# Optimization experiments

Measured on AMD Instinct MI355X. Metric: run time of the kernel, lower is better.

The kernel has to match this reference:

```python
import jax, jax.numpy as jnp
import numpy as np

N, E, H = 50000, 800000, 128
NUM_NC = 40
NUM_LAYERS = 3


def setup_inputs() -> dict:
    key = jax.random.key(0)
    ks = jax.random.split(key, 16)
    s = 1.0 / np.sqrt(H)
    inp = {
        "x": jax.random.normal(ks[0], (N, H), jnp.float32),
        "edge_index": jax.random.randint(ks[1], (2, E), 0, N, jnp.int64),
        "na_alphas": 0.001 * jax.random.normal(ks[2], (3, 4), jnp.float32),
        "sc_alphas": 0.001 * jax.random.normal(ks[3], (2, 2), jnp.float32),
        "la_alphas": 0.001 * jax.random.normal(ks[4], (1, 3), jnp.float32),
        "lin1_W": s * jax.random.normal(ks[5], (H, H), jnp.float32),
        "lin1_b": jnp.zeros((H,), jnp.float32),
        "gcn_W": s * jax.random.normal(ks[6], (3, H, H), jnp.float32),
        "gcn_b": jnp.zeros((3, H), jnp.float32),
        "sage_Ws": s * jax.random.normal(ks[7], (3, H, H), jnp.float32),
        "sage_Wn": s * jax.random.normal(ks[8], (3, H, H), jnp.float32),
        "gin_W": s * jax.random.normal(ks[9], (3, H, H), jnp.float32),
        "gin_b": jnp.zeros((3, H), jnp.float32),
        "gin_eps": jnp.zeros((3,), jnp.float32),
        "gat_W": s * jax.random.normal(ks[10], (3, H, H), jnp.float32),
        "gat_as": s * jax.random.normal(ks[11], (3, H), jnp.float32),
        "gat_ad": s * jax.random.normal(ks[12], (3, H), jnp.float32),
        "nc_W": s * jax.random.normal(ks[13], (NUM_NC, H), jnp.float32),
        "nc_b": jnp.zeros((NUM_NC,), jnp.float32),
    }
    return inp


def _gcn(x, src, dst, deg_inv_sqrt, W, b):
    h = x @ W.T + b                           # [N, H]
    norm = deg_inv_sqrt[src] * deg_inv_sqrt[dst]
    msg = h[src] * norm[:, None]              # [E, H] gather
    return jax.ops.segment_sum(msg, dst, num_segments=N)


def _sage(x, src, dst, deg, Ws, Wn):
    agg = jax.ops.segment_sum(x[src], dst, num_segments=N) / jnp.maximum(deg, 1.0)[:, None]
    return x @ Ws.T + agg @ Wn.T


def _gin(x, src, dst, W, b, eps):
    agg = jax.ops.segment_sum(x[src], dst, num_segments=N)
    return ((1.0 + eps) * x + agg) @ W.T + b


def _gat(x, src, dst, W, a_s, a_d):
    h = x @ W.T                               # [N, H]
    logits = jax.nn.leaky_relu((h @ a_s)[src] + (h @ a_d)[dst], 0.2)  # [E]
    m = jax.ops.segment_max(logits, dst, num_segments=N)
    e = jnp.exp(logits - m[dst])
    z = jax.ops.segment_sum(e, dst, num_segments=N)
    alpha = e / (z[dst] + 1e-16)
    return jax.ops.segment_sum(alpha[:, None] * h[src], dst, num_segments=N)


def _na_mixed(x, w, src, dst, deg, dis, l, gcn_W, gcn_b, sage_Ws, sage_Wn,
              gin_W, gin_b, gin_eps, gat_W, gat_as, gat_ad):
    # sum_i w_i * elu(op_i(x, edge_index))
    o0 = _gcn(x, src, dst, dis, gcn_W[l], gcn_b[l])
    o1 = _sage(x, src, dst, deg, sage_Ws[l], sage_Wn[l])
    o2 = _gin(x, src, dst, gin_W[l], gin_b[l], gin_eps[l])
    o3 = _gat(x, src, dst, gat_W[l], gat_as[l], gat_ad[l])
    return (w[0] * jax.nn.elu(o0) + w[1] * jax.nn.elu(o1)
            + w[2] * jax.nn.elu(o2) + w[3] * jax.nn.elu(o3))


def reference(x, edge_index, na_alphas, sc_alphas, la_alphas, lin1_W, lin1_b,
              gcn_W, gcn_b, sage_Ws, sage_Wn, gin_W, gin_b, gin_eps,
              gat_W, gat_as, gat_ad, nc_W, nc_b):
    src, dst = edge_index[0], edge_index[1]
    deg = jax.ops.segment_sum(jnp.ones((E,), x.dtype), dst, num_segments=N)
    dis = jnp.where(deg > 0, 1.0 / jnp.sqrt(jnp.maximum(deg, 1.0)), 0.0)

    na_w = jax.nn.softmax(na_alphas, axis=-1)   # [3, 4]
    sc_w = jax.nn.softmax(sc_alphas, axis=-1)   # [2, 2] (none, skip)
    la_w = jax.nn.softmax(la_alphas, axis=-1)   # [1, 3]

    h = x @ lin1_W.T + lin1_b                   # dropout: eval mode -> identity
    xs = []
    cur = h
    for l in range(NUM_LAYERS):
        cur = _na_mixed(cur, na_w[l], src, dst, deg, dis, l, gcn_W, gcn_b,
                        sage_Ws, sage_Wn, gin_W, gin_b, gin_eps,
                        gat_W, gat_as, gat_ad)
        xs.append(cur)
    x1, x2, x3 = xs

    # fix_last=True: x4 = (x3, sc0(x1), sc1(x2)); SC ops = {none->0, skip->id}
    t = jnp.stack([x3, sc_w[0, 1] * x1, sc_w[1, 1] * x2], axis=0)  # [3, N, H]

    # layer aggregator: sum_i w_i * relu(op_i(tuple)); ops = {max, mean, sum}
    x5 = (la_w[0, 0] * jax.nn.relu(jnp.max(t, axis=0))
          + la_w[0, 1] * jax.nn.relu(jnp.mean(t, axis=0))
          + la_w[0, 2] * jax.nn.relu(jnp.sum(t, axis=0)))

    return x5 @ nc_W.T + nc_b                   # [N, NUM_NC]
```

## Files before the change

kernel.cpp:

```cpp
#include <hip/hip_runtime.h>
#include <hip/hip_bf16.h>

typedef unsigned short u16;
typedef unsigned int u32;
typedef __attribute__((ext_vector_type(8))) short short8;
typedef __attribute__((ext_vector_type(4))) float f32x4;
typedef __attribute__((ext_vector_type(2))) float f32x2;

#define HD 128

__device__ inline float b2f(u16 u){ u32 v = ((u32)u) << 16; return __uint_as_float(v); }
__device__ inline u16 f2b(float f){
  u32 u = __float_as_uint(f);
  u32 r = (u + 0x7fffu + ((u >> 16) & 1u)) >> 16;
  return (u16)r;
}
__device__ inline u32 pack2(float a, float b){
  __hip_bfloat162 h = __float22bfloat162_rn(make_float2(a, b));
  union { __hip_bfloat162 h; u32 u; } c; c.h = h; return c.u;
}
__device__ inline float lo2f(u32 w){ return b2f((u16)(w & 0xffff)); }
__device__ inline float hi2f(u32 w){ return b2f((u16)(w >> 16)); }
__device__ inline float eluf(float x){ return x > 0.f ? x : __expf(x) - 1.f; }
__device__ inline float reluf(float x){ return x > 0.f ? x : 0.f; }
__device__ inline float sane(float x){
  if (!(x == x)) return 0.f;
  return fminf(fmaxf(x, -1e30f), 1e30f);
}
__device__ inline u32 fenc(float f){ u32 u = __float_as_uint(f); return (u & 0x80000000u) ? ~u : (u | 0x80000000u); }
__device__ inline float fdec(u32 u){ return __uint_as_float((u & 0x80000000u) ? (u & 0x7fffffffu) : ~u); }
__device__ __forceinline__ void async16(const u16* g, u16* l){
  __builtin_amdgcn_global_load_lds((const __attribute__((address_space(1))) void*)g,
                                   (__attribute__((address_space(3))) void*)l, 16, 0, 0);
}

__global__ void k_small(const float* __restrict__ na_a, const float* __restrict__ sc_a,
                        const float* __restrict__ la_a, const float* __restrict__ gatW,
                        const float* __restrict__ gat_as, const float* __restrict__ gat_ad,
                        const float* __restrict__ gin_eps, float* __restrict__ sm,
                        u32* __restrict__ maxs)
{
  int t = threadIdx.x;
  if (t < 3) maxs[t] = 0u;
  if (t == 0){
    for (int l = 0; l < 3; l++){
      float a[4]; float mx = -1e30f;
      for (int i = 0; i < 4; i++){ a[i] = na_a[l*4+i]; mx = fmaxf(mx, a[i]); }
      float ssum = 0.f;
      for (int i = 0; i < 4; i++){ a[i] = __expf(a[i]-mx); ssum += a[i]; }
      for (int i = 0; i < 4; i++) sm[l*4+i] = a[i]/ssum;
    }
    for (int r = 0; r < 2; r++){
      float a0 = sc_a[r*2], a1 = sc_a[r*2+1];
      float mx = fmaxf(a0,a1);
      float e0 = __expf(a0-mx), e1 = __expf(a1-mx);
      sm[12+r] = e1/(e0+e1);
    }
    {
      float a0=la_a[0], a1=la_a[1], a2=la_a[2];
      float mx = fmaxf(fmaxf(a0,a1),a2);
      float e0=__expf(a0-mx), e1=__expf(a1-mx), e2=__expf(a2-mx);
      float ssum = e0+e1+e2;
      sm[14]=e0/ssum; sm[15]=e1/ssum; sm[16]=e2/ssum;
    }
    for (int l=0;l<3;l++) sm[17+l] = 1.f + gin_eps[l];
  }
  if (t < 128){
    for (int l=0;l<3;l++){
      float a1=0.f, a2=0.f;
      for (int k=0;k<128;k++){
        float wv = gatW[l*16384 + k*128 + t];
        a1 = fmaf(wv, gat_as[l*128+k], a1);
        a2 = fmaf(wv, gat_ad[l*128+k], a2);
      }
      sm[32  + l*128 + t] = a1;
      sm[416 + l*128 + t] = a2;
    }
  }
}

__device__ __forceinline__ uint4 cvt8(const float* __restrict__ p){
  float4 v0 = *(const float4*)p;
  float4 v1 = *(const float4*)(p + 4);
  uint4 o;
  o.x = pack2(v0.x, v0.y);
  o.y = pack2(v0.z, v0.w);
  o.z = pack2(v1.x, v1.y);
  o.w = pack2(v1.z, v1.w);
  return o;
}
__global__ void k_wcvt(const float* __restrict__ lin1W, const float* __restrict__ gcnW,
                       const float* __restrict__ Ws, const float* __restrict__ Wn,
                       const float* __restrict__ ginW, const float* __restrict__ gatW,
                       u16* __restrict__ wsb)
{
  int i = blockIdx.x*256 + threadIdx.x;
  if (i >= 32768) return;
  int m = i >> 11;
  int j = i & 2047;
  int r = j >> 4, c = j & 15;
  const float* src;
  if (m == 0)       src = lin1W;
  else if (m < 4)   src = gcnW + (m-1)*16384;
  else if (m < 7)   src = Ws   + (m-4)*16384;
  else if (m < 10)  src = Wn   + (m-7)*16384;
  else if (m < 13)  src = ginW + (m-10)*16384;
  else              src = gatW + (m-13)*16384;
  int dj = r*16 + (c ^ (r & 15));
  *(uint4*)(wsb + ((size_t)m*2048 + dj)*8) = cvt8(src + r*HD + c*8);
}

__global__ void k_count(const int* __restrict__ ei, int E, int* __restrict__ cnt){
  int e = blockIdx.x*256 + threadIdx.x;
  if (e < E) atomicAdd(&cnt[ei[E + e]], 1);
}

__global__ void k_scan1(const int* __restrict__ cnt, int Nn, int* __restrict__ bsum){
  __shared__ int red[256];
  int b = blockIdx.x, t = threadIdx.x;
  int base = b*1024 + t*4;
  int s = 0;
  #pragma unroll
  for (int k = 0; k < 4; k++){ int i = base + k; if (i < Nn) s += cnt[i]; }
  red[t] = s; __syncthreads();
  for (int off = 128; off; off >>= 1){
    if (t < off) red[t] += red[t + off];
    __syncthreads();
  }
  if (t == 0) bsum[b] = red[0];
}

__global__ void k_scan2(const int* __restrict__ bsum, int nb,
                        int* __restrict__ boffs, int* __restrict__ rowptr, int Nn){
  __shared__ int sc[1024];
  int t = threadIdx.x;
  int own = (t < nb) ? bsum[t] : 0;
  sc[t] = own;
  __syncthreads();
  for (int off = 1; off < 1024; off <<= 1){
    int add = (t >= off) ? sc[t - off] : 0;
    __syncthreads();
    sc[t] += add;
    __syncthreads();
  }
  if (t < nb) boffs[t] = sc[t] - own;
  if (t == 1023) rowptr[Nn] = sc[1023];
}

__global__ void k_scan3(const int* __restrict__ cnt, const int* __restrict__ boffs, int Nn,
                        int* __restrict__ rowptr, int* __restrict__ cursor,
                        float4* __restrict__ nd){
  __shared__ int red[256];
  int b = blockIdx.x, t = threadIdx.x;
  int base = b*1024 + t*4;
  int c[4]; int s = 0;
  #pragma unroll
  for (int k = 0; k < 4; k++){ int i = base + k; c[k] = (i < Nn) ? cnt[i] : 0; s += c[k]; }
  red[t] = s; __syncthreads();
  for (int off = 1; off < 256; off <<= 1){
    int add = (t >= off) ? red[t - off] : 0;
    __syncthreads();
    red[t] += add;
    __syncthreads();
  }
  int run = red[t] - s + boffs[b];
  #pragma unroll
  for (int k = 0; k < 4; k++){
    int i = base + k;
    if (i < Nn){
      rowptr[i] = run; cursor[i] = run;
      float f = (float)c[k];
      nd[i].z = c[k] > 0 ? 1.f/sqrtf(f) : 0.f;
      nd[i].w = 1.f/fmaxf(f, 1.f);
      run += c[k];
    }
  }
}

__global__ void k_fill(const int* __restrict__ ei, int E,
                       int* __restrict__ cursor, int* __restrict__ csr){
  int e = blockIdx.x*256 + threadIdx.x;
  if (e < E){
    int sv = ei[e], dv = ei[E + e];
    int pos = atomicAdd(&cursor[dv], 1);
    csr[pos] = sv;
  }
}

__global__ __launch_bounds__(256)
void k_agg(const u16* __restrict__ X, const int* __restrict__ rowptr, const int* __restrict__ csr,
           const float4* __restrict__ nd, const float* __restrict__ sm,
           const u32* __restrict__ maxs, int layer, int Nn,
           u16* __restrict__ Qb, u16* __restrict__ Pm, u16* __restrict__ Gb, u16* __restrict__ Rb,
           float* __restrict__ b0)
{
  int wv = blockIdx.x*4 + (threadIdx.x >> 6);
  if (wv >= Nn) return;
  int lane = threadIdx.x & 63;
  int g = lane >> 4, t = lane & 15;
  int beg = rowptr[wv], end = rowptr[wv+1];
  float4 ndw = nd[wv];
  float dval = ndw.y;
  float bnd = fdec(maxs[layer]) + dval;
  float mloc = fmaxf(bnd, 0.2f*bnd);
  f32x2 p2[4], q2[4], r2[4];
  #pragma unroll
  for (int k = 0; k < 4; k++){ p2[k] = (f32x2){0.f,0.f}; q2[k] = (f32x2){0.f,0.f}; r2[k] = (f32x2){0.f,0.f}; }
  float z = 0.f, qd = 0.f;
  int e = beg + g;
  for (; e + 4 < end; e += 8){
    int sv0 = csr[e], sv1 = csr[e+4];
    float4 n0 = nd[sv0], n1 = nd[sv1];
    uint4 xv0 = *(const uint4*)(X + (size_t)sv0*HD + (t ^ (sv0 & 15))*8);
    uint4 xv1 = *(const uint4*)(X + (size_t)sv1*HD + (t ^ (sv1 & 15))*8);
    float s0 = n0.x + dval, s1 = n1.x + dval;
    float lg0 = fmaxf(s0, 0.2f*s0);
    float lg1 = fmaxf(s1, 0.2f*s1);
    float ew0 = __expf(lg0 - mloc), ew1 = __expf(lg1 - mloc);
    u32 a0[4] = {xv0.x, xv0.y, xv0.z, xv0.w};
    u32 a1[4] = {xv1.x, xv1.y, xv1.z, xv1.w};
    f32x2 d0 = {n0.z, n0.z}, d1 = {n1.z, n1.z};
    f32x2 e0 = {ew0, ew0},   e1v = {ew1, ew1};
    #pragma unroll
    for (int k = 0; k < 4; k++){
      f32x2 xf0 = {lo2f(a0[k]), hi2f(a0[k])};
      f32x2 xf1 = {lo2f(a1[k]), hi2f(a1[k])};
      p2[k] += xf0 + xf1;
      q2[k] = __builtin_elementwise_fma(xf0, d0, q2[k]);
      q2[k] = __builtin_elementwise_fma(xf1, d1, q2[k]);
      r2[k] = __builtin_elementwise_fma(xf0, e0, r2[k]);
      r2[k] = __builtin_elementwise_fma(xf1, e1v, r2[k]);
    }
    z += ew0 + ew1; qd += n0.z + n1.z;
  }
  if (e < end){
    int sv = csr[e];
    float4 n0 = nd[sv];
    uint4 xv = *(const uint4*)(X + (size_t)sv*HD + (t ^ (sv & 15))*8);
    float s = n0.x + dval;
    float lg = fmaxf(s, 0.2f*s);
    float ew = __expf(lg - mloc);
    u32 a0[4] = {xv.x, xv.y, xv.z, xv.w};
    f32x2 d0 = {n0.z, n0.z}, e0 = {ew, ew};
    #pragma unroll
    for (int k = 0; k < 4; k++){
      f32x2 xf = {lo2f(a0[k]), hi2f(a0[k])};
      p2[k] += xf;
      q2[k] = __builtin_elementwise_fma(xf, d0, q2[k]);
      r2[k] = __builtin_elementwise_fma(xf, e0, r2[k]);
    }
    z += ew; qd += n0.z;
  }
  #pragma unroll
  for (int off = 16; off <= 32; off <<= 1){
    #pragma unroll
    for (int k = 0; k < 4; k++){
      p2[k].x += __shfl_xor(p2[k].x, off); p2[k].y += __shfl_xor(p2[k].y, off);
      q2[k].x += __shfl_xor(q2[k].x, off); q2[k].y += __shfl_xor(q2[k].y, off);
      r2[k].x += __shfl_xor(r2[k].x, off); r2[k].y += __shfl_xor(r2[k].y, off);
    }
    z  += __shfl_xor(z, off);
    qd += __shfl_xor(qd, off);
  }
  if (g == 0){
    float disv = ndw.z, dinvv = ndw.w;
    float zinv = 1.f/(z + 1e-16f);
    float e1 = sm[17 + layer];
    int tch = t ^ (wv & 15);
    size_t o = (size_t)wv*HD + tch*8;
    uint4 xo = *(const uint4*)(X + o);
    u32 ax[4] = {xo.x, xo.y, xo.z, xo.w};
    uint4 qo, po, go, ro;
    u32* qp = (u32*)&qo; u32* pp = (u32*)&po; u32* gp = (u32*)&go; u32* rp = (u32*)&ro;
    #pragma unroll
    for (int k = 0; k < 4; k++){
      float x0 = lo2f(ax[k]), x1 = hi2f(ax[k]);
      qp[k] = pack2(disv*q2[k].x, disv*q2[k].y);
      pp[k] = pack2(dinvv*p2[k].x, dinvv*p2[k].y);
      gp[k] = pack2(fmaf(e1, x0, p2[k].x), fmaf(e1, x1, p2[k].y));
      rp[k] = pack2(zinv*r2[k].x, zinv*r2[k].y);
    }
    *(uint4*)(Qb + o) = qo;
    *(uint4*)(Pm + o) = po;
    *(uint4*)(Gb + o) = go;
    *(uint4*)(Rb + o) = ro;
    if (t == 0) b0[wv] = disv*qd;
  }
}

__device__ __forceinline__ void stageB_async(u16* lds, const u16* __restrict__ w, int tid){
  int lane = tid & 63, wave = tid >> 6;
  #pragma unroll
  for (int i = 0; i < 8; i++){
    int cb = wave*64 + 256*i;
    async16(w + (size_t)(cb + lane)*8, lds + (size_t)cb*8);
  }
}
__device__ __forceinline__ void stageA64_async(u16* lds, const u16* __restrict__ src,
                                               int mbase, int Nn, int tid){
  int lane = tid & 63, wave = tid >> 6;
  #pragma unroll
  for (int i = 0; i < 4; i++){
    int cb = wave*64 + 256*i;
    int gr = mbase + ((cb + lane) >> 4);
    if (gr < Nn)
      async16(src + ((size_t)mbase*16 + cb + lane)*8, lds + (size_t)cb*8);
  }
}
__device__ __forceinline__ void stageA64_f32(u16* lds, const float* __restrict__ src,
                                             int mbase, int Nn, int tid){
  #pragma unroll
  for (int i = 0; i < 4; i++){
    int chunk = tid + 256*i;
    int r = chunk >> 4;
    int c = chunk & 15;
    uint4 v = {0u,0u,0u,0u};
    int gr = mbase + r;
    if (gr < Nn) v = cvt8(src + (size_t)gr*HD + c*8);
    *(uint4*)(lds + (r*16 + (c ^ (r & 15)))*8) = v;
  }
}
__device__ __forceinline__ void mfma_tile64(const u16* Als, const u16* Bls,
                                            int m0, int lane, f32x4 acc[8]){
  int quad = lane >> 4, lr = lane & 15;
  #pragma unroll
  for (int ks = 0; ks < 4; ks++){
    int q = ks*4 + quad;
    short8 a, b[8];
    int row = m0 + lr;
    a = *(const short8*)(Als + (row*16 + (q ^ lr))*8);
    #pragma unroll
    for (int ct = 0; ct < 8; ct++){
      int brow = ct*16 + lr;
      b[ct] = *(const short8*)(Bls + (brow*16 + (q ^ lr))*8);
    }
    #pragma unroll
    for (int ct = 0; ct < 8; ct++)
      acc[ct] = __builtin_amdgcn_mfma_f32_16x16x32_bf16(a, b[ct], acc[ct], 0, 0, 0);
  }
}

__global__ __launch_bounds__(256,3)
void k_gemm1(const float* __restrict__ A, const u16* __restrict__ Wb, const float* __restrict__ bias,
             const float* __restrict__ sm, float4* __restrict__ nd, u32* __restrict__ maxs,
             int Nn, u16* __restrict__ out)
{
  __shared__ __align__(16) u16 Als[64*128];
  __shared__ __align__(16) u16 Bls[128*128];
  __shared__ float mred[4];
  int tid = threadIdx.x;
  int lane = tid & 63, wave = tid >> 6;
  int m0 = wave*16, mbase = blockIdx.x*64;
  int quad = lane >> 4, lr = lane & 15;
  f32x4 acc[8];
  #pragma unroll
  for (int ct=0;ct<8;ct++) acc[ct] = (f32x4){0.f,0.f,0.f,0.f};
  stageB_async(Bls, Wb, tid);
  stageA64_f32(Als, A, mbase, Nn, tid);
  __syncthreads();
  mfma_tile64(Als, Bls, m0, lane, acc);
  #pragma unroll
  for (int ct=0;ct<8;ct++){
    float bc = bias[ct*16+lr];
    #pragma unroll
    for (int r=0;r<4;r++) acc[ct][r] = sane(acc[ct][r] + bc);
  }
  #pragma unroll
  for (int ct=0;ct<8;ct++){
    int c2 = ct*2 + (lr >> 3);
    #pragma unroll
    for (int r=0;r<4;r++){
      int grow = mbase + m0 + quad*4 + r;
      if (grow < Nn) out[(size_t)grow*HD + (c2 ^ (grow & 15))*8 + (lr & 7)] = f2b(acc[ct][r]);
    }
  }
  {
    const float* wsv = sm + 32;
    const float* wdv = sm + 416;
    float sp[4] = {0.f,0.f,0.f,0.f}, dp[4] = {0.f,0.f,0.f,0.f};
    #pragma unroll
    for (int ct=0;ct<8;ct++){
      float wsc = wsv[ct*16+lr], wdc = wdv[ct*16+lr];
      #pragma unroll
      for (int r=0;r<4;r++){
        sp[r] = fmaf(acc[ct][r], wsc, sp[r]);
        dp[r] = fmaf(acc[ct][r], wdc, dp[r]);
      }
    }
    #pragma unroll
    for (int off=1; off<16; off<<=1)
      #pragma unroll
      for (int r=0;r<4;r++){ sp[r] += __shfl_xor(sp[r], off); dp[r] += __shfl_xor(dp[r], off); }
    float ms = -3.4e38f;
    #pragma unroll
    for (int r=0;r<4;r++){
      int grow = mbase + m0 + quad*4 + r;
      if (grow < Nn){
        ms = fmaxf(ms, sp[r]);
        if (lr == 0) *(float2*)&nd[grow] = make_float2(sp[r], dp[r]);
      }
    }
    ms = fmaxf(ms, __shfl_xor(ms, 16));
    ms = fmaxf(ms, __shfl_xor(ms, 32));
    if (lane == 0) mred[wave] = ms;
    __syncthreads();
    if (tid == 0){
      float m = fmaxf(fmaxf(mred[0],mred[1]), fmaxf(mred[2],mred[3]));
      atomicMax(maxs + 0, fenc(m));
    }
  }
}

__global__ __launch_bounds__(256,3)
void k_layer3(const u16* __restrict__ X, const u16* __restrict__ Qb,
              const u16* __restrict__ Pm, const u16* __restrict__ Gb, const u16* __restrict__ Rb,
              float4* __restrict__ nd, const float* __restrict__ b0,
              const u16* __restrict__ wsb,
              const float* __restrict__ gcnB, const float* __restrict__ ginB,
              const float* __restrict__ sm, u32* __restrict__ maxs,
              int layer, int Nn, u16* __restrict__ out)
{
  __shared__ __align__(16) u16 At[64*128];
  __shared__ __align__(16) u16 Bt[128*128];
  __shared__ float mred[4];
  int tid = threadIdx.x;
  int lane = tid & 63, wave = tid >> 6;
  int m0 = wave*16, mbase = blockIdx.x*64;
  int quad = lane >> 4, lr = lane & 15;
  float w0 = sm[layer*4+0], w1 = sm[layer*4+1], w2 = sm[layer*4+2], w3 = sm[layer*4+3];
  const u16* gcnWb = wsb + (size_t)(1  + layer)*16384;
  const u16* WsWb  = wsb + (size_t)(4  + layer)*16384;
  const u16* WnWb  = wsb + (size_t)(7  + layer)*16384;
  const u16* ginWb = wsb + (size_t)(10 + layer)*16384;
  const u16* gatWb = wsb + (size_t)(13 + layer)*16384;

  f32x4 mix[8];
  f32x4 acc[8];
  float b0r[4];
  #pragma unroll
  for (int r=0;r<4;r++){
    int grow = mbase + m0 + quad*4 + r;
    b0r[r] = (grow < Nn) ? b0[grow] : 0.f;
  }

  stageB_async(Bt, gcnWb, tid);
  stageA64_async(At, Qb, mbase, Nn, tid);
  __syncthreads();
  #pragma unroll
  for (int ct=0;ct<8;ct++) acc[ct] = (f32x4){0.f,0.f,0.f,0.f};
  mfma_tile64(At, Bt, m0, lane, acc);
  {
    float gb[8];
    #pragma unroll
    for (int ct=0;ct<8;ct++) gb[ct] = gcnB[layer*HD + ct*16+lr];
    #pragma unroll
    for (int ct=0;ct<8;ct++)
      #pragma unroll
      for (int r=0;r<4;r++)
        mix[ct][r] = w0 * eluf(acc[ct][r] + b0r[r]*gb[ct]);
  }
  __syncthreads();

  stageB_async(Bt, WsWb, tid);
  stageA64_async(At, X, mbase, Nn, tid);
  __syncthreads();
  #pragma unroll
  for (int ct=0;ct<8;ct++) acc[ct] = (f32x4){0.f,0.f,0.f,0.f};
  mfma_tile64(At, Bt, m0, lane, acc);
  __syncthreads();
  stageB_async(Bt, WnWb, tid);
  stageA64_async(At, Pm, mbase, Nn, tid);
  __syncthreads();
  mfma_tile64(At, Bt, m0, lane, acc);
  #pragma unroll
  for (int ct=0;ct<8;ct++)
    #pragma unroll
    for (int r=0;r<4;r++)
      mix[ct][r] += w1 * eluf(acc[ct][r]);
  __syncthreads();

  stageB_async(Bt, ginWb, tid);
  stageA64_async(At, Gb, mbase, Nn, tid);
  __syncthreads();
  #pragma unroll
  for (int ct=0;ct<8;ct++) acc[ct] = (f32x4){0.f,0.f,0.f,0.f};
  mfma_tile64(At, Bt, m0, lane, acc);
  {
    float gib[8];
    #pragma unroll
    for (int ct=0;ct<8;ct++) gib[ct] = ginB[layer*HD + ct*16+lr];
    #pragma unroll
    for (int ct=0;ct<8;ct++)
      #pragma unroll
      for (int r=0;r<4;r++)
        mix[ct][r] += w2 * eluf(acc[ct][r] + gib[ct]);
  }
  __syncthreads();

  stageB_async(Bt, gatWb, tid);
  stageA64_async(At, Rb, mbase, Nn, tid);
  __syncthreads();
  #pragma unroll
  for (int ct=0;ct<8;ct++) acc[ct] = (f32x4){0.f,0.f,0.f,0.f};
  mfma_tile64(At, Bt, m0, lane, acc);
  #pragma unroll
  for (int ct=0;ct<8;ct++)
    #pragma unroll
    for (int r=0;r<4;r++)
      mix[ct][r] = sane(mix[ct][r] + w3 * eluf(acc[ct][r]));

  #pragma unroll
  for (int ct=0;ct<8;ct++){
    int c2 = ct*2 + (lr >> 3);
    #pragma unroll
    for (int r=0;r<4;r++){
      int grow = mbase + m0 + quad*4 + r;
      if (grow < Nn) out[(size_t)grow*HD + (c2 ^ (grow & 15))*8 + (lr & 7)] = f2b(mix[ct][r]);
    }
  }
  if (layer < 2){
    const float* wsv = sm + 32  + (layer+1)*128;
    const float* wdv = sm + 416 + (layer+1)*128;
    float sp[4] = {0.f,0.f,0.f,0.f}, dp[4] = {0.f,0.f,0.f,0.f};
    #pragma unroll
    for (int ct=0;ct<8;ct++){
      float wsc = wsv[ct*16+lr], wdc = wdv[ct*16+lr];
      #pragma unroll
      for (int r=0;r<4;r++){
        sp[r] = fmaf(mix[ct][r], wsc, sp[r]);
        dp[r] = fmaf(mix[ct][r], wdc, dp[r]);
      }
    }
    #pragma unroll
    for (int off=1; off<16; off<<=1)
      #pragma unroll
      for (int r=0;r<4;r++){ sp[r] += __shfl_xor(sp[r], off); dp[r] += __shfl_xor(dp[r], off); }
    float ms = -3.4e38f;
    #pragma unroll
    for (int r=0;r<4;r++){
      int grow = mbase + m0 + quad*4 + r;
      if (grow < Nn){
        ms = fmaxf(ms, sp[r]);
        if (lr == 0) *(float2*)&nd[grow] = make_float2(sp[r], dp[r]);
      }
    }
    ms = fmaxf(ms, __shfl_xor(ms, 16));
    ms = fmaxf(ms, __shfl_xor(ms, 32));
    if (lane == 0) mred[wave] = ms;
    __syncthreads();
    if (tid == 0){
      float m = fmaxf(fmaxf(mred[0],mred[1]), fmaxf(mred[2],mred[3]));
      atomicMax(maxs + layer + 1, fenc(m));
    }
  }
}

__global__ __launch_bounds__(256)
void k_nc(const u16* __restrict__ X1, const u16* __restrict__ X2, const u16* __restrict__ X3,
          const float* __restrict__ W, const float* __restrict__ bias,
          const float* __restrict__ sm, int Nn, float* __restrict__ out)
{
  __shared__ __align__(16) u16 xs[32*136];
  __shared__ __align__(16) float wn[40*132];
  __shared__ float bs[40];
  int t = threadIdx.x;
  int nb = blockIdx.x*32;
  float c1 = sm[12], c2 = sm[13], la0 = sm[14], la1 = sm[15], la2 = sm[16];
  #pragma unroll
  for (int i = 0; i < 2; i++){
    int chunk = t + 256*i;
    int r = chunk >> 4, c = chunk & 15;
    uint4 v = {0u,0u,0u,0u};
    int gr = nb + r;
    if (gr < Nn){
      size_t o = (size_t)gr*HD + ((c ^ (gr & 15))*8);
      uint4 u1 = *(const uint4*)(X1 + o);
      uint4 u2 = *(const uint4*)(X2 + o);
      uint4 u3 = *(const uint4*)(X3 + o);
      u32* u1p = (u32*)&u1; u32* u2p = (u32*)&u2; u32* u3p = (u32*)&u3; u32* vp = (u32*)&v;
      #pragma unroll
      for (int k = 0; k < 4; k++){
        float o0, o1;
        {
          float a1 = lo2f(u1p[k]), a2 = lo2f(u2p[k]), a3 = lo2f(u3p[k]);
          float t0 = a3, t1 = c1*a1, t2 = c2*a2;
          float smm = t0 + t1 + t2;
          float mx = fmaxf(fmaxf(t0,t1),t2);
          o0 = la0*reluf(mx) + la1*reluf(smm*(1.f/3.f)) + la2*reluf(smm);
        }
        {
          float a1 = hi2f(u1p[k]), a2 = hi2f(u2p[k]), a3 = hi2f(u3p[k]);
          float t0 = a3, t1 = c1*a1, t2 = c2*a2;
          float smm = t0 + t1 + t2;
          float mx = fmaxf(fmaxf(t0,t1),t2);
          o1 = la0*reluf(mx) + la1*reluf(smm*(1.f/3.f)) + la2*reluf(smm);
        }
        vp[k] = pack2(sane(o0), sane(o1));
      }
    }
    *(uint4*)(xs + r*136 + c*8) = v;
  }
  #pragma unroll
  for (int i = 0; i < 5; i++){
    int chunk = t + 256*i;
    int r = chunk >> 5, c = chunk & 31;
    *(float4*)(wn + r*132 + c*4) = *(const float4*)(W + r*HD + c*4);
  }
  if (t < 40) bs[t] = bias[t];
  __syncthreads();
  int nl = t >> 3, cg = t & 7;
  float acc[5];
  #pragma unroll
  for (int j = 0; j < 5; j++) acc[j] = bs[cg + 8*j];
  for (int k = 0; k < 128; k++){
    float xv = b2f(xs[nl*136 + k]);
    #pragma unroll
    for (int j = 0; j < 5; j++)
      acc[j] = fmaf(xv, wn[(cg + 8*j)*132 + k], acc[j]);
  }
  int gr = nb + nl;
  if (gr < Nn){
    #pragma unroll
    for (int j = 0; j < 5; j++)
      out[(size_t)gr*40 + cg + 8*j] = sane(acc[j]);
  }
}

extern "C" void kernel_launch(void* const* d_in, const int* in_sizes, int n_in,
                              void* d_out, int out_size, void* d_ws, size_t ws_size,
                              hipStream_t stream)
{
  (void)n_in; (void)out_size; (void)ws_size;
  const int N = in_sizes[0] / HD;
  const int E = in_sizes[1] / 2;
  const float* x      = (const float*)d_in[0];
  const int*   ei     = (const int*)d_in[1];
  const float* na_a   = (const float*)d_in[2];
  const float* sc_a   = (const float*)d_in[3];
  const float* la_a   = (const float*)d_in[4];
  const float* lin1W  = (const float*)d_in[5];
  const float* lin1b  = (const float*)d_in[6];
  const float* gcnW   = (const float*)d_in[7];
  const float* gcnB   = (const float*)d_in[8];
  const float* sageWs = (const float*)d_in[9];
  const float* sageWn = (const float*)d_in[10];
  const float* ginW   = (const float*)d_in[11];
  const float* ginB   = (const float*)d_in[12];
  const float* ginE   = (const float*)d_in[13];
  const float* gatW   = (const float*)d_in[14];
  const float* gatAs  = (const float*)d_in[15];
  const float* gatAd  = (const float*)d_in[16];
  const float* ncW    = (const float*)d_in[17];
  const float* ncB    = (const float*)d_in[18];

  char* base = (char*)d_ws;
  size_t off = 0;
  auto alloc = [&](size_t b) -> void* {
    void* p = base + off;
    off += (b + 255) & ~(size_t)255;
    return p;
  };
  const int NB = (N + 1023) / 1024;
  float*  smalls = (float*)alloc(4096);
  u32*    maxs   = (u32*)alloc(256);
  int*    cnt    = (int*)alloc((size_t)N*4);
  int*    rowptr = (int*)alloc(((size_t)N+1)*4);
  int*    cursor = (int*)alloc((size_t)N*4);
  int*    bsum   = (int*)alloc(4096);
  int*    boffs  = (int*)alloc(4096);
  float4* nd     = (float4*)alloc((size_t)N*16);
  float*  b0     = (float*)alloc((size_t)N*4);
  int*    csr    = (int*)alloc((size_t)E*4);
  u16*    wsb    = (u16*)alloc((size_t)16*16384*2);
  u16*    xh     = (u16*)alloc((size_t)N*HD*2);
  u16*    x1     = (u16*)alloc((size_t)N*HD*2);
  u16*    x2     = (u16*)alloc((size_t)N*HD*2);
  u16*    Qb     = (u16*)alloc((size_t)N*HD*2);
  u16*    Pm     = (u16*)alloc((size_t)N*HD*2);
  u16*    Gb     = (u16*)alloc((size_t)N*HD*2);
  u16*    Rb     = (u16*)alloc((size_t)N*HD*2);

  hipMemsetAsync(cnt, 0, (size_t)N*4, stream);
  k_small<<<1,128,0,stream>>>(na_a, sc_a, la_a, gatW, gatAs, gatAd, ginE, smalls, maxs);
  k_wcvt<<<128,256,0,stream>>>(lin1W, gcnW, sageWs, sageWn, ginW, gatW, wsb);
  int ebl = (E + 255)/256;
  k_count<<<ebl,256,0,stream>>>(ei, E, cnt);
  k_scan1<<<NB,256,0,stream>>>(cnt, N, bsum);
  k_scan2<<<1,1024,0,stream>>>(bsum, NB, boffs, rowptr, N);
  k_scan3<<<NB,256,0,stream>>>(cnt, boffs, N, rowptr, cursor, nd);
  k_fill<<<ebl,256,0,stream>>>(ei, E, cursor, csr);
  int gbl64 = (N + 63)/64;
  k_gemm1<<<gbl64,256,0,stream>>>(x, wsb, lin1b, smalls, nd, maxs, N, xh);
  const u16* xc = xh;
  u16* outs[3] = {x1, x2, xh};
  int wbl = (N + 3)/4;
  for (int l = 0; l < 3; l++){
    k_agg<<<wbl,256,0,stream>>>(xc, rowptr, csr, nd, smalls, maxs, l, N, Qb, Pm, Gb, Rb, b0);
    k_layer3<<<gbl64,256,0,stream>>>(xc, Qb, Pm, Gb, Rb, nd, b0, wsb,
                                     gcnB, ginB, smalls, maxs, l, N, outs[l]);
    xc = outs[l];
  }
  int ncbl = (N + 31)/32;
  k_nc<<<ncbl,256,0,stream>>>(x1, x2, xh, ncW, ncB, smalls, N, (float*)d_out);
}
```

Measured before the change: 512.8 us.

## Gather neighbor features in FP8 and derive GIN aggregate from mean buffer

The producing kernels now also write an FP8 copy of each node's features, and the edge aggregation gathers these 8-byte rows instead of 16-byte bf16 rows, halving the dominant random-gather traffic. The GIN input buffer is removed. Its matmul is rebuilt in the layer kernel as deg times (mean-agg @ W) plus (1+eps) times (x @ W), which costs one extra MFMA tile pass but drops one buffer write and read. FP8 gathers lower accuracy of all three aggregations, and the GIN sum is now recovered from a bf16-rounded mean multiplied by the degree.

```diff
diff --git a/kernel.cpp b/kernel.cpp
--- a/kernel.cpp
+++ b/kernel.cpp
@@ -2,6 +2,7 @@
 #include <hip/hip_bf16.h>
 
 typedef unsigned short u16;
+typedef unsigned char u8;
 typedef unsigned int u32;
 typedef __attribute__((ext_vector_type(8))) short short8;
 typedef __attribute__((ext_vector_type(4))) float f32x4;
@@ -29,6 +30,9 @@
 }
 __device__ inline u32 fenc(float f){ u32 u = __float_as_uint(f); return (u & 0x80000000u) ? ~u : (u | 0x80000000u); }
 __device__ inline float fdec(u32 u){ return __uint_as_float((u & 0x80000000u) ? (u & 0x7fffffffu) : ~u); }
+__device__ inline u8 f2fp8(float v){
+  return (u8)__builtin_amdgcn_cvt_pk_fp8_f32(v, v, 0, false);
+}
 __device__ __forceinline__ void async16(const u16* g, u16* l){
   __builtin_amdgcn_global_load_lds((const __attribute__((address_space(1))) void*)g,
                                    (__attribute__((address_space(3))) void*)l, 16, 0, 0);
@@ -188,10 +192,9 @@
 }
 
 __global__ __launch_bounds__(256)
-void k_agg(const u16* __restrict__ X, const int* __restrict__ rowptr, const int* __restrict__ csr,
-           const float4* __restrict__ nd, const float* __restrict__ sm,
-           const u32* __restrict__ maxs, int layer, int Nn,
-           u16* __restrict__ Qb, u16* __restrict__ Pm, u16* __restrict__ Gb, u16* __restrict__ Rb,
+void k_agg(const u8* __restrict__ Xf8, const int* __restrict__ rowptr, const int* __restrict__ csr,
+           const float4* __restrict__ nd, const u32* __restrict__ maxs, int layer, int Nn,
+           u16* __restrict__ Qb, u16* __restrict__ Pm, u16* __restrict__ Rb,
            float* __restrict__ b0)
 {
   int wv = blockIdx.x*4 + (threadIdx.x >> 6);
@@ -211,43 +214,51 @@
   for (; e + 4 < end; e += 8){
     int sv0 = csr[e], sv1 = csr[e+4];
     float4 n0 = nd[sv0], n1 = nd[sv1];
-    uint4 xv0 = *(const uint4*)(X + (size_t)sv0*HD + (t ^ (sv0 & 15))*8);
-    uint4 xv1 = *(const uint4*)(X + (size_t)sv1*HD + (t ^ (sv1 & 15))*8);
+    uint2 xv0 = *(const uint2*)(Xf8 + (size_t)sv0*HD + ((t ^ (sv0 & 15))<<3));
+    uint2 xv1 = *(const uint2*)(Xf8 + (size_t)sv1*HD + ((t ^ (sv1 & 15))<<3));
     float s0 = n0.x + dval, s1 = n1.x + dval;
     float lg0 = fmaxf(s0, 0.2f*s0);
     float lg1 = fmaxf(s1, 0.2f*s1);
     float ew0 = __expf(lg0 - mloc), ew1 = __expf(lg1 - mloc);
-    u32 a0[4] = {xv0.x, xv0.y, xv0.z, xv0.w};
-    u32 a1[4] = {xv1.x, xv1.y, xv1.z, xv1.w};
+    f32x2 x0c[4], x1c[4];
+    x0c[0] = __builtin_amdgcn_cvt_pk_f32_fp8(xv0.x, false);
+    x0c[1] = __builtin_amdgcn_cvt_pk_f32_fp8(xv0.x, true);
+    x0c[2] = __builtin_amdgcn_cvt_pk_f32_fp8(xv0.y, false);
+    x0c[3] = __builtin_amdgcn_cvt_pk_f32_fp8(xv0.y, true);
+    x1c[0] = __builtin_amdgcn_cvt_pk_f32_fp8(xv1.x, false);
+    x1c[1] = __builtin_amdgcn_cvt_pk_f32_fp8(xv1.x, true);
+    x1c[2] = __builtin_amdgcn_cvt_pk_f32_fp8(xv1.y, false);
+    x1c[3] = __builtin_amdgcn_cvt_pk_f32_fp8(xv1.y, true);
     f32x2 d0 = {n0.z, n0.z}, d1 = {n1.z, n1.z};
     f32x2 e0 = {ew0, ew0},   e1v = {ew1, ew1};
     #pragma unroll
     for (int k = 0; k < 4; k++){
-      f32x2 xf0 = {lo2f(a0[k]), hi2f(a0[k])};
-      f32x2 xf1 = {lo2f(a1[k]), hi2f(a1[k])};
-      p2[k] += xf0 + xf1;
-      q2[k] = __builtin_elementwise_fma(xf0, d0, q2[k]);
-      q2[k] = __builtin_elementwise_fma(xf1, d1, q2[k]);
-      r2[k] = __builtin_elementwise_fma(xf0, e0, r2[k]);
-      r2[k] = __builtin_elementwise_fma(xf1, e1v, r2[k]);
+      p2[k] += x0c[k] + x1c[k];
+      q2[k] = __builtin_elementwise_fma(x0c[k], d0, q2[k]);
+      q2[k] = __builtin_elementwise_fma(x1c[k], d1, q2[k]);
+      r2[k] = __builtin_elementwise_fma(x0c[k], e0, r2[k]);
+      r2[k] = __builtin_elementwise_fma(x1c[k], e1v, r2[k]);
     }
     z += ew0 + ew1; qd += n0.z + n1.z;
   }
   if (e < end){
     int sv = csr[e];
     float4 n0 = nd[sv];
-    uint4 xv = *(const uint4*)(X + (size_t)sv*HD + (t ^ (sv & 15))*8);
+    uint2 xv = *(const uint2*)(Xf8 + (size_t)sv*HD + ((t ^ (sv & 15))<<3));
     float s = n0.x + dval;
     float lg = fmaxf(s, 0.2f*s);
     float ew = __expf(lg - mloc);
-    u32 a0[4] = {xv.x, xv.y, xv.z, xv.w};
+    f32x2 xc[4];
+    xc[0] = __builtin_amdgcn_cvt_pk_f32_fp8(xv.x, false);
+    xc[1] = __builtin_amdgcn_cvt_pk_f32_fp8(xv.x, true);
+    xc[2] = __builtin_amdgcn_cvt_pk_f32_fp8(xv.y, false);
+    xc[3] = __builtin_amdgcn_cvt_pk_f32_fp8(xv.y, true);
     f32x2 d0 = {n0.z, n0.z}, e0 = {ew, ew};
     #pragma unroll
     for (int k = 0; k < 4; k++){
-      f32x2 xf = {lo2f(a0[k]), hi2f(a0[k])};
-      p2[k] += xf;
-      q2[k] = __builtin_elementwise_fma(xf, d0, q2[k]);
-      r2[k] = __builtin_elementwise_fma(xf, e0, r2[k]);
+      p2[k] += xc[k];
+      q2[k] = __builtin_elementwise_fma(xc[k], d0, q2[k]);
+      r2[k] = __builtin_elementwise_fma(xc[k], e0, r2[k]);
     }
     z += ew; qd += n0.z;
   }
@@ -265,24 +276,18 @@
   if (g == 0){
     float disv = ndw.z, dinvv = ndw.w;
     float zinv = 1.f/(z + 1e-16f);
-    float e1 = sm[17 + layer];
     int tch = t ^ (wv & 15);
     size_t o = (size_t)wv*HD + tch*8;
-    uint4 xo = *(const uint4*)(X + o);
-    u32 ax[4] = {xo.x, xo.y, xo.z, xo.w};
-    uint4 qo, po, go, ro;
-    u32* qp = (u32*)&qo; u32* pp = (u32*)&po; u32* gp = (u32*)&go; u32* rp = (u32*)&ro;
+    uint4 qo, po, ro;
+    u32* qp = (u32*)&qo; u32* pp = (u32*)&po; u32* rp = (u32*)&ro;
     #pragma unroll
     for (int k = 0; k < 4; k++){
-      float x0 = lo2f(ax[k]), x1 = hi2f(ax[k]);
       qp[k] = pack2(disv*q2[k].x, disv*q2[k].y);
       pp[k] = pack2(dinvv*p2[k].x, dinvv*p2[k].y);
-      gp[k] = pack2(fmaf(e1, x0, p2[k].x), fmaf(e1, x1, p2[k].y));
       rp[k] = pack2(zinv*r2[k].x, zinv*r2[k].y);
     }
     *(uint4*)(Qb + o) = qo;
     *(uint4*)(Pm + o) = po;
-    *(uint4*)(Gb + o) = go;
     *(uint4*)(Rb + o) = ro;
     if (t == 0) b0[wv] = disv*qd;
   }
@@ -343,7 +348,7 @@
 __global__ __launch_bounds__(256,3)
 void k_gemm1(const float* __restrict__ A, const u16* __restrict__ Wb, const float* __restrict__ bias,
              const float* __restrict__ sm, float4* __restrict__ nd, u32* __restrict__ maxs,
-             int Nn, u16* __restrict__ out)
+             int Nn, u16* __restrict__ out, u8* __restrict__ Xs8)
 {
   __shared__ __align__(16) u16 Als[64*128];
   __shared__ __align__(16) u16 Bls[128*128];
@@ -371,7 +376,11 @@
     #pragma unroll
     for (int r=0;r<4;r++){
       int grow = mbase + m0 + quad*4 + r;
-      if (grow < Nn) out[(size_t)grow*HD + (c2 ^ (grow & 15))*8 + (lr & 7)] = f2b(acc[ct][r]);
+      if (grow < Nn){
+        size_t rb = (size_t)grow*HD + ((c2 ^ (grow & 15))<<3);
+        out[rb + (lr & 7)] = f2b(acc[ct][r]);
+        Xs8[rb + (lr & 7)] = f2fp8(acc[ct][r]);
+      }
     }
   }
   {
@@ -413,12 +422,13 @@
 
 __global__ __launch_bounds__(256,3)
 void k_layer3(const u16* __restrict__ X, const u16* __restrict__ Qb,
-              const u16* __restrict__ Pm, const u16* __restrict__ Gb, const u16* __restrict__ Rb,
+              const u16* __restrict__ Pm, const u16* __restrict__ Rb,
               float4* __restrict__ nd, const float* __restrict__ b0,
+              const int* __restrict__ cnt,
               const u16* __restrict__ wsb,
               const float* __restrict__ gcnB, const float* __restrict__ ginB,
               const float* __restrict__ sm, u32* __restrict__ maxs,
-              int layer, int Nn, u16* __restrict__ out)
+              int layer, int Nn, u16* __restrict__ out, u8* __restrict__ Xs8)
 {
   __shared__ __align__(16) u16 At[64*128];
   __shared__ __align__(16) u16 Bt[128*128];
@@ -428,6 +438,7 @@
   int m0 = wave*16, mbase = blockIdx.x*64;
   int quad = lane >> 4, lr = lane & 15;
   float w0 = sm[layer*4+0], w1 = sm[layer*4+1], w2 = sm[layer*4+2], w3 = sm[layer*4+3];
+  float e1 = sm[17 + layer];
   const u16* gcnWb = wsb + (size_t)(1  + layer)*16384;
   const u16* WsWb  = wsb + (size_t)(4  + layer)*16384;
   const u16* WnWb  = wsb + (size_t)(7  + layer)*16384;
@@ -435,20 +446,21 @@
   const u16* gatWb = wsb + (size_t)(13 + layer)*16384;
 
   f32x4 mix[8];
-  f32x4 acc[8];
-  float b0r[4];
+  f32x4 a1[8], a2[8];
+  float b0r[4], md[4];
   #pragma unroll
   for (int r=0;r<4;r++){
     int grow = mbase + m0 + quad*4 + r;
     b0r[r] = (grow < Nn) ? b0[grow] : 0.f;
+    md[r]  = (grow < Nn) ? fmaxf((float)cnt[grow], 1.f) : 1.f;
   }
 
   stageB_async(Bt, gcnWb, tid);
   stageA64_async(At, Qb, mbase, Nn, tid);
   __syncthreads();
   #pragma unroll
-  for (int ct=0;ct<8;ct++) acc[ct] = (f32x4){0.f,0.f,0.f,0.f};
-  mfma_tile64(At, Bt, m0, lane, acc);
+  for (int ct=0;ct<8;ct++) a1[ct] = (f32x4){0.f,0.f,0.f,0.f};
+  mfma_tile64(At, Bt, m0, lane, a1);
   {
     float gb[8];
     #pragma unroll
@@ -457,7 +469,7 @@
     for (int ct=0;ct<8;ct++)
       #pragma unroll
       for (int r=0;r<4;r++)
-        mix[ct][r] = w0 * eluf(acc[ct][r] + b0r[r]*gb[ct]);
+        mix[ct][r] = w0 * eluf(a1[ct][r] + b0r[r]*gb[ct]);
   }
   __syncthreads();
 
@@ -465,26 +477,33 @@
   stageA64_async(At, X, mbase, Nn, tid);
   __syncthreads();
   #pragma unroll
-  for (int ct=0;ct<8;ct++) acc[ct] = (f32x4){0.f,0.f,0.f,0.f};
-  mfma_tile64(At, Bt, m0, lane, acc);
-  __syncthreads();
+  for (int ct=0;ct<8;ct++) a1[ct] = (f32x4){0.f,0.f,0.f,0.f};
+  mfma_tile64(At, Bt, m0, lane, a1);
+  __syncthreads();
+
   stageB_async(Bt, WnWb, tid);
   stageA64_async(At, Pm, mbase, Nn, tid);
   __syncthreads();
-  mfma_tile64(At, Bt, m0, lane, acc);
+  mfma_tile64(At, Bt, m0, lane, a1);
   #pragma unroll
   for (int ct=0;ct<8;ct++)
     #pragma unroll
     for (int r=0;r<4;r++)
-      mix[ct][r] += w1 * eluf(acc[ct][r]);
+      mix[ct][r] += w1 * eluf(a1[ct][r]);
   __syncthreads();
 
   stageB_async(Bt, ginWb, tid);
-  stageA64_async(At, Gb, mbase, Nn, tid);
-  __syncthreads();
-  #pragma unroll
-  for (int ct=0;ct<8;ct++) acc[ct] = (f32x4){0.f,0.f,0.f,0.f};
-  mfma_tile64(At, Bt, m0, lane, acc);
+  __syncthreads();
+  #pragma unroll
+  for (int ct=0;ct<8;ct++) a2[ct] = (f32x4){0.f,0.f,0.f,0.f};
+  mfma_tile64(At, Bt, m0, lane, a2);
+  __syncthreads();
+
+  stageA64_async(At, X, mbase, Nn, tid);
+  __syncthreads();
+  #pragma unroll
+  for (int ct=0;ct<8;ct++) a1[ct] = (f32x4){0.f,0.f,0.f,0.f};
+  mfma_tile64(At, Bt, m0, lane, a1);
   {
     float gib[8];
     #pragma unroll
@@ -493,7 +512,7 @@
     for (int ct=0;ct<8;ct++)
       #pragma unroll
       for (int r=0;r<4;r++)
-        mix[ct][r] += w2 * eluf(acc[ct][r] + gib[ct]);
+        mix[ct][r] += w2 * eluf(fmaf(e1, a1[ct][r], fmaf(md[r], a2[ct][r], gib[ct])));
   }
   __syncthreads();
 
@@ -501,13 +520,13 @@
   stageA64_async(At, Rb, mbase, Nn, tid);
   __syncthreads();
   #pragma unroll
-  for (int ct=0;ct<8;ct++) acc[ct] = (f32x4){0.f,0.f,0.f,0.f};
-  mfma_tile64(At, Bt, m0, lane, acc);
+  for (int ct=0;ct<8;ct++) a1[ct] = (f32x4){0.f,0.f,0.f,0.f};
+  mfma_tile64(At, Bt, m0, lane, a1);
   #pragma unroll
   for (int ct=0;ct<8;ct++)
     #pragma unroll
     for (int r=0;r<4;r++)
-      mix[ct][r] = sane(mix[ct][r] + w3 * eluf(acc[ct][r]));
+      mix[ct][r] = sane(mix[ct][r] + w3 * eluf(a1[ct][r]));
 
   #pragma unroll
   for (int ct=0;ct<8;ct++){
@@ -515,7 +534,11 @@
     #pragma unroll
     for (int r=0;r<4;r++){
       int grow = mbase + m0 + quad*4 + r;
-      if (grow < Nn) out[(size_t)grow*HD + (c2 ^ (grow & 15))*8 + (lr & 7)] = f2b(mix[ct][r]);
+      if (grow < Nn){
+        size_t rb = (size_t)grow*HD + ((c2 ^ (grow & 15))<<3);
+        out[rb + (lr & 7)] = f2b(mix[ct][r]);
+        if (layer < 2) Xs8[rb + (lr & 7)] = f2fp8(mix[ct][r]);
+      }
     }
   }
   if (layer < 2){
@@ -677,8 +700,8 @@
   u16*    x2     = (u16*)alloc((size_t)N*HD*2);
   u16*    Qb     = (u16*)alloc((size_t)N*HD*2);
   u16*    Pm     = (u16*)alloc((size_t)N*HD*2);
-  u16*    Gb     = (u16*)alloc((size_t)N*HD*2);
   u16*    Rb     = (u16*)alloc((size_t)N*HD*2);
+  u8*     Xs8    = (u8*)alloc((size_t)N*HD);
 
   hipMemsetAsync(cnt, 0, (size_t)N*4, stream);
   k_small<<<1,128,0,stream>>>(na_a, sc_a, la_a, gatW, gatAs, gatAd, ginE, smalls, maxs);
@@ -690,14 +713,14 @@
   k_scan3<<<NB,256,0,stream>>>(cnt, boffs, N, rowptr, cursor, nd);
   k_fill<<<ebl,256,0,stream>>>(ei, E, cursor, csr);
   int gbl64 = (N + 63)/64;
-  k_gemm1<<<gbl64,256,0,stream>>>(x, wsb, lin1b, smalls, nd, maxs, N, xh);
+  k_gemm1<<<gbl64,256,0,stream>>>(x, wsb, lin1b, smalls, nd, maxs, N, xh, Xs8);
   const u16* xc = xh;
   u16* outs[3] = {x1, x2, xh};
   int wbl = (N + 3)/4;
   for (int l = 0; l < 3; l++){
-    k_agg<<<wbl,256,0,stream>>>(xc, rowptr, csr, nd, smalls, maxs, l, N, Qb, Pm, Gb, Rb, b0);
-    k_layer3<<<gbl64,256,0,stream>>>(xc, Qb, Pm, Gb, Rb, nd, b0, wsb,
-                                     gcnB, ginB, smalls, maxs, l, N, outs[l]);
+    k_agg<<<wbl,256,0,stream>>>(Xs8, rowptr, csr, nd, maxs, l, N, Qb, Pm, Rb, b0);
+    k_layer3<<<gbl64,256,0,stream>>>(xc, Qb, Pm, Rb, nd, b0, cnt, wsb,
+                                     gcnB, ginB, smalls, maxs, l, N, outs[l], Xs8);
     xc = outs[l];
   }
   int ncbl = (N + 31)/32;
```

After: 558.2 us. 8.9% more time.
